# Performance work log

Measured on AMD Instinct MI355X. Metric: run time of the kernel, lower is better.

## Reference

```python
import jax, jax.numpy as jnp
import numpy as np

D_QKV = 64

def setup_inputs() -> dict:
    key = jax.random.key(0)
    k1, k2, k3, k4 = jax.random.split(key, 4)
    B, T, D = 4, 2048, 1024
    x = jax.random.normal(k1, (B, T, D), dtype=jnp.float32)
    Wq = jax.random.normal(k2, (D, D_QKV), dtype=jnp.float32) * (D ** -0.5)
    Wk = jax.random.normal(k3, (D, D_QKV), dtype=jnp.float32) * (D ** -0.5)
    Wv = jax.random.normal(k4, (D, D_QKV), dtype=jnp.float32) * (D ** -0.5)
    return {"x": x, "Wq": Wq, "Wk": Wk, "Wv": Wv}

def reference(x, Wq, Wk, Wv):
    # x: [B, T, D]; single-head causal attention with head dim d_qkv
    T = x.shape[1]
    q = jnp.einsum("btd,de->bte", x, Wq)  # [B, T, d]
    k = jnp.einsum("btd,de->bte", x, Wk)
    v = jnp.einsum("btd,de->bte", x, Wv)
    scores = jnp.einsum("bqe,bke->bqk", q, k) / (D_QKV ** 0.5)  # [B, T, T]
    causal = jnp.tril(jnp.ones((T, T), dtype=bool))
    scores = jnp.where(causal, scores, -jnp.inf)
    attn = jax.nn.softmax(scores, axis=2)
    return jnp.einsum("bqk,bke->bqe", attn, v)  # [B, T, d]
```

## Files before the change

### kernel.cpp

```cpp
#include <hip/hip_runtime.h>
#include <hip/hip_bf16.h>

typedef __hip_bfloat16 bf16;
typedef __bf16 bf16x8 __attribute__((ext_vector_type(8)));
typedef float f32x4 __attribute__((ext_vector_type(4)));
typedef unsigned short u16x8 __attribute__((ext_vector_type(8)));

#define B_SZ   4
#define T_SEQ  2048
#define D_IN   1024
#define D_QKV  64
#define BT     (B_SZ * T_SEQ)
#define PSTR   72

#define GLD_LDS(gp, lp) __builtin_amdgcn_global_load_lds(                     \
    (const __attribute__((address_space(1))) void*)(gp),                      \
    (__attribute__((address_space(3))) void*)(lp), 16, 0, 0)

__global__ __launch_bounds__(256) void wt_prep(
    const float* __restrict__ Wq, const float* __restrict__ Wk,
    const float* __restrict__ Wv, bf16* __restrict__ wt)
{
    __shared__ float ws[64 * 65];
    const int bx = blockIdx.x;
    const int m  = bx >> 4;
    const int k0 = (bx & 15) << 6;
    const float* W = (m == 0) ? Wq : (m == 1) ? Wk : Wv;
    const int tid = threadIdx.x;
    #pragma unroll
    for (int i = 0; i < 16; ++i) {
        const int idx = i * 256 + tid;
        const int kk = idx >> 6, nn = idx & 63;
        ws[kk * 65 + nn] = W[(size_t)(k0 + kk) * D_QKV + nn];
    }
    __syncthreads();
    const int n = tid >> 2, kq = (tid & 3) << 4;
    bf16 tmp[16];
    #pragma unroll
    for (int j = 0; j < 16; ++j)
        tmp[j] = __float2bfloat16(ws[(kq + j) * 65 + n]);
    uint4* dst = (uint4*)(wt + (size_t)(m * 64 + n) * D_IN + k0 + kq);
    dst[0] = ((uint4*)tmp)[0];
    dst[1] = ((uint4*)tmp)[1];
}

__global__ __launch_bounds__(256) void qkv_proj_mfma(
    const float* __restrict__ x, const bf16* __restrict__ wt,
    bf16* __restrict__ qb, bf16* __restrict__ kb, bf16* __restrict__ vt)
{
    __shared__ uint4 As[2][1024];
    __shared__ uint4 Bs[2][768];

    const int tid  = threadIdx.x;
    const int wave = tid >> 6;
    const int lane = tid & 63;
    const int col  = lane & 15;
    const int quad = lane >> 4;
    const int bx   = blockIdx.x;
    const int m0   = (bx >> 1) * 64;
    const int ng   = bx & 1;

    f32x4 acc[6];
    #pragma unroll
    for (int i = 0; i < 6; ++i) acc[i] = (f32x4){0.f, 0.f, 0.f, 0.f};

    auto stage = [&](int it, int buf) {
        const int k0 = it * 64;
        #pragma unroll
        for (int j = 0; j < 7; ++j) {
            const int s = wave + j * 4;
            if (s < 16) {
                const int c = s * 64 + lane;
                const int r = c >> 4;
                const int ccl = ((c & 15) - r) & 15;
                const float* g = x + (size_t)(m0 + r) * D_IN + k0 + ccl * 4;
                GLD_LDS(g, &As[buf][s * 64]);
            } else {
                const int bs = s - 16;
                const int c = bs * 64 + lane;
                const int n = c >> 3;
                const int ccl = ((c & 7) - n) & 7;
                const bf16* g = wt + (size_t)(ng * 96 + n) * D_IN + k0 + ccl * 8;
                GLD_LDS(g, &Bs[buf][bs * 64]);
            }
        }
    };

    stage(0, 0);
    const int r = wave * 16 + col;
    #pragma unroll 1
    for (int it = 0; it < 16; ++it) {
        __syncthreads();
        if (it + 1 < 16) stage(it + 1, (it + 1) & 1);
        const float4* Ac = (const float4*)As[it & 1];
        const uint4*  Bc = Bs[it & 1];
        #pragma unroll
        for (int s = 0; s < 2; ++s) {
            const int ca = s * 8 + quad * 2;
            const float4 a0 = Ac[r * 16 + ((ca + r) & 15)];
            const float4 a1 = Ac[r * 16 + ((ca + 1 + r) & 15)];
            const bf16x8 af = (bf16x8){(__bf16)a0.x, (__bf16)a0.y, (__bf16)a0.z, (__bf16)a0.w,
                                       (__bf16)a1.x, (__bf16)a1.y, (__bf16)a1.z, (__bf16)a1.w};
            #pragma unroll
            for (int i = 0; i < 6; ++i) {
                const int n = i * 16 + col;
                const bf16x8 bfr = __builtin_bit_cast(bf16x8,
                    Bc[n * 8 + ((s * 4 + quad + n) & 7)]);
                acc[i] = __builtin_amdgcn_mfma_f32_16x16x32_bf16(af, bfr, acc[i], 0, 0, 0);
            }
        }
    }

    const int bb = m0 >> 11;
    const int tl = m0 & (T_SEQ - 1);
    #pragma unroll
    for (int i = 0; i < 6; ++i) {
        const int n = ng * 96 + i * 16 + col;
        #pragma unroll
        for (int rr = 0; rr < 4; ++rr) {
            const int row = m0 + wave * 16 + quad * 4 + rr;
            const bf16 vq = __float2bfloat16(acc[i][rr]);
            if (n < 64)       qb[(size_t)row * D_QKV + n] = vq;
            else if (n < 128) kb[(size_t)row * D_QKV + (n - 64)] = vq;
            else              vt[(size_t)bb * D_QKV * T_SEQ + (size_t)(n - 128) * T_SEQ
                                 + (tl + wave * 16 + quad * 4 + rr)] = vq;
        }
    }
}

__global__ __launch_bounds__(256) void attn_kernel(
    const bf16* __restrict__ qb, const bf16* __restrict__ kb,
    const bf16* __restrict__ vt, float* __restrict__ Op, float* __restrict__ lp)
{
    __shared__ uint4 Ks[2][512];
    __shared__ uint4 Vs[2][512];
    __shared__ unsigned short plds[4 * 16 * PSTR];

    const int tid  = threadIdx.x;
    const int wave = tid >> 6;
    const int lane = tid & 63;
    const int col  = lane & 15;
    const int quad = lane >> 4;
    const int bx   = blockIdx.x;
    const int tile    = (bx < 256) ? (127 - (bx >> 2)) : ((bx - 256) >> 2);
    const int quarter = bx & 3;
    const int b    = tile >> 5;
    const int qloc = (tile & 31) * 64;
    const int nch  = (tile & 31) + 1;

    const bf16* kbp = kb + (size_t)b * T_SEQ * D_QKV;
    const bf16* vtp = vt + (size_t)b * D_QKV * T_SEQ;
    const uint4* q4 = (const uint4*)(qb + (size_t)b * T_SEQ * D_QKV);

    const bf16x8 aq0 = __builtin_bit_cast(bf16x8, q4[(qloc + wave * 16 + col) * 8 + quad]);
    const bf16x8 aq1 = __builtin_bit_cast(bf16x8, q4[(qloc + wave * 16 + col) * 8 + 4 + quad]);

    f32x4 o[4];
    float ls[4];
    #pragma unroll
    for (int dt = 0; dt < 4; ++dt) o[dt] = (f32x4){0.f, 0.f, 0.f, 0.f};
    #pragma unroll
    for (int rr = 0; rr < 4; ++rr) ls[rr] = 0.f;

    unsigned short* pl = plds + wave * 16 * PSTR;
    const u16x8* p8 = (const u16x8*)pl;

    auto stage = [&](int c, int buf) {
        const int kb0 = c * 64;
        #pragma unroll
        for (int j = 0; j < 4; ++j) {
            const int s = wave + j * 4;
            if (s < 8) {
                const int ch = s * 64 + lane;
                const int key = ch >> 3;
                const int ccl = ((ch & 7) - key) & 7;
                const bf16* g = kbp + (size_t)(kb0 + key) * D_QKV + ccl * 8;
                GLD_LDS(g, &Ks[buf][s * 64]);
            } else {
                const int vs = s - 8;
                const int ch = vs * 64 + lane;
                const int d = ch >> 3;
                const int ccl = ((ch & 7) - d) & 7;
                const bf16* g = vtp + (size_t)d * T_SEQ + kb0 + ccl * 8;
                GLD_LDS(g, &Vs[buf][vs * 64]);
            }
        }
    };

    if (quarter < nch) stage(quarter, 0);
    int i = 0;
    for (int c = quarter; c < nch; c += 4, ++i) {
        __syncthreads();
        if (c + 4 < nch) stage(c + 4, (i + 1) & 1);
        const uint4* Kc = Ks[i & 1];
        const uint4* Vc = Vs[i & 1];

        f32x4 sc[4];
        #pragma unroll
        for (int nt = 0; nt < 4; ++nt) {
            const int kp = nt * 16 + col;
            const bf16x8 bk0 = __builtin_bit_cast(bf16x8, Kc[kp * 8 + ((quad + kp) & 7)]);
            const bf16x8 bk1 = __builtin_bit_cast(bf16x8, Kc[kp * 8 + ((4 + quad + kp) & 7)]);
            sc[nt] = (f32x4){0.f, 0.f, 0.f, 0.f};
            sc[nt] = __builtin_amdgcn_mfma_f32_16x16x32_bf16(aq0, bk0, sc[nt], 0, 0, 0);
            sc[nt] = __builtin_amdgcn_mfma_f32_16x16x32_bf16(aq1, bk1, sc[nt], 0, 0, 0);
        }

        if (c == nch - 1) {
            #pragma unroll
            for (int nt = 0; nt < 4; ++nt) {
                const int kp = c * 64 + nt * 16 + col;
                #pragma unroll
                for (int rr = 0; rr < 4; ++rr)
                    if (kp > qloc + wave * 16 + quad * 4 + rr) sc[nt][rr] = -INFINITY;
            }
        }

        #pragma unroll
        for (int nt = 0; nt < 4; ++nt) {
            #pragma unroll
            for (int rr = 0; rr < 4; ++rr) {
                const float pv = __expf(sc[nt][rr] * 0.125f);
                ls[rr] += pv;
                pl[(quad * 4 + rr) * PSTR + nt * 16 + col] =
                    __builtin_bit_cast(unsigned short, __float2bfloat16(pv));
            }
        }

        const bf16x8 pa0 = __builtin_bit_cast(bf16x8, p8[col * 9 + quad]);
        const bf16x8 pa1 = __builtin_bit_cast(bf16x8, p8[col * 9 + 4 + quad]);

        #pragma unroll
        for (int dt = 0; dt < 4; ++dt) {
            const int dp = dt * 16 + col;
            const bf16x8 bv0 = __builtin_bit_cast(bf16x8, Vc[dp * 8 + ((quad + dp) & 7)]);
            const bf16x8 bv1 = __builtin_bit_cast(bf16x8, Vc[dp * 8 + ((4 + quad + dp) & 7)]);
            o[dt] = __builtin_amdgcn_mfma_f32_16x16x32_bf16(pa0, bv0, o[dt], 0, 0, 0);
            o[dt] = __builtin_amdgcn_mfma_f32_16x16x32_bf16(pa1, bv1, o[dt], 0, 0, 0);
        }
    }

    #pragma unroll
    for (int rr = 0; rr < 4; ++rr) {
        #pragma unroll
        for (int msk = 1; msk < 16; msk <<= 1)
            ls[rr] += __shfl_xor(ls[rr], msk);
    }

    const int pbase = (tile * 4 + quarter) * 64 + wave * 16;
    #pragma unroll
    for (int dt = 0; dt < 4; ++dt)
        #pragma unroll
        for (int rr = 0; rr < 4; ++rr)
            Op[(size_t)(pbase + quad * 4 + rr) * D_QKV + dt * 16 + col] = o[dt][rr];
    if (col == 0) {
        #pragma unroll
        for (int rr = 0; rr < 4; ++rr)
            lp[pbase + quad * 4 + rr] = ls[rr];
    }
}

__global__ __launch_bounds__(256) void combine_kernel(
    const float* __restrict__ Op, const float* __restrict__ lp,
    float* __restrict__ out)
{
    const int idx = blockIdx.x * 256 + threadIdx.x;
    const int qg = idx >> 6, d = idx & 63;
    const int tile = qg >> 6, qq = qg & 63;
    float s = 0.f, l = 0.f;
    #pragma unroll
    for (int k = 0; k < 4; ++k) {
        s += Op[(size_t)((tile * 4 + k) * 64 + qq) * D_QKV + d];
        l += lp[(tile * 4 + k) * 64 + qq];
    }
    out[(size_t)qg * D_QKV + d] = s / l;
}

extern "C" void kernel_launch(void* const* d_in, const int* in_sizes, int n_in,
                              void* d_out, int out_size, void* d_ws, size_t ws_size,
                              hipStream_t stream) {
    const float* x  = (const float*)d_in[0];
    const float* Wq = (const float*)d_in[1];
    const float* Wk = (const float*)d_in[2];
    const float* Wv = (const float*)d_in[3];
    float* out = (float*)d_out;

    char* ws = (char*)d_ws;
    bf16*  qb = (bf16*)(ws);
    bf16*  kb = (bf16*)(ws + (1u << 20));
    bf16*  vt = (bf16*)(ws + (2u << 20));
    bf16*  wt = (bf16*)(ws + (3u << 20));
    float* Op = (float*)(ws + (4u << 20));
    float* lp = (float*)(ws + (12u << 20));

    wt_prep<<<48, 256, 0, stream>>>(Wq, Wk, Wv, wt);
    qkv_proj_mfma<<<256, 256, 0, stream>>>(x, wt, qb, kb, vt);
    attn_kernel<<<512, 256, 0, stream>>>(qb, kb, vt, Op, lp);
    combine_kernel<<<2048, 256, 0, stream>>>(Op, lp, out);
}
```

Baseline: 110.1 us.

## Split-K QKV projection with 128-row tiles and 128-query attention tiles

The QKV projection now uses 128-row tiles covering all 192 output columns and splits the K dimension into four blocks. This avoids loading x twice, and the fp32 partials are summed in a new combine_qkv kernel that also writes the transposed V. The attention kernel processes two 64-query subtiles per block, reusing each K/V chunk load for both and halving the grid to 256 blocks. In exchange it adds an extra kernel launch, writes and reads about 25 MB of partials, and drops the previous longest-first tile ordering, which risks load imbalance.

```diff
diff --git a/kernel.cpp b/kernel.cpp
--- a/kernel.cpp
+++ b/kernel.cpp
@@ -12,6 +12,7 @@
 #define D_QKV  64
 #define BT     (B_SZ * T_SEQ)
 #define PSTR   72
+#define QS     ((size_t)BT * 192)
 
 #define GLD_LDS(gp, lp) __builtin_amdgcn_global_load_lds(                     \
     (const __attribute__((address_space(1))) void*)(gp),                      \
@@ -46,10 +47,10 @@
 
 __global__ __launch_bounds__(256) void qkv_proj_mfma(
     const float* __restrict__ x, const bf16* __restrict__ wt,
-    bf16* __restrict__ qb, bf16* __restrict__ kb, bf16* __restrict__ vt)
-{
-    __shared__ uint4 As[2][1024];
-    __shared__ uint4 Bs[2][768];
+    float* __restrict__ Pp)
+{
+    __shared__ uint4 As[2][2048];
+    __shared__ uint4 Bs[2][1536];
 
     const int tid  = threadIdx.x;
     const int wave = tid >> 6;
@@ -57,74 +58,113 @@
     const int col  = lane & 15;
     const int quad = lane >> 4;
     const int bx   = blockIdx.x;
-    const int m0   = (bx >> 1) * 64;
-    const int ng   = bx & 1;
-
-    f32x4 acc[6];
-    #pragma unroll
-    for (int i = 0; i < 6; ++i) acc[i] = (f32x4){0.f, 0.f, 0.f, 0.f};
+    const int m0   = (bx >> 2) * 128;
+    const int kq   = bx & 3;
+
+    f32x4 acc[2][12];
+    #pragma unroll
+    for (int mt = 0; mt < 2; ++mt)
+        #pragma unroll
+        for (int i = 0; i < 12; ++i) acc[mt][i] = (f32x4){0.f, 0.f, 0.f, 0.f};
 
     auto stage = [&](int it, int buf) {
-        const int k0 = it * 64;
-        #pragma unroll
-        for (int j = 0; j < 7; ++j) {
+        const int k0 = kq * 256 + it * 64;
+        #pragma unroll
+        for (int j = 0; j < 14; ++j) {
             const int s = wave + j * 4;
-            if (s < 16) {
-                const int c = s * 64 + lane;
-                const int r = c >> 4;
-                const int ccl = ((c & 15) - r) & 15;
-                const float* g = x + (size_t)(m0 + r) * D_IN + k0 + ccl * 4;
+            if (s < 32) {
+                const int o = s * 64 + lane;
+                const int r = o >> 4;
+                const int ch = ((o & 15) - r) & 15;
+                const float* g = x + (size_t)(m0 + r) * D_IN + k0 + ch * 4;
                 GLD_LDS(g, &As[buf][s * 64]);
             } else {
-                const int bs = s - 16;
-                const int c = bs * 64 + lane;
-                const int n = c >> 3;
-                const int ccl = ((c & 7) - n) & 7;
-                const bf16* g = wt + (size_t)(ng * 96 + n) * D_IN + k0 + ccl * 8;
-                GLD_LDS(g, &Bs[buf][bs * 64]);
+                const int o = (s - 32) * 64 + lane;
+                const int n = o >> 3;
+                const int ch = ((o & 7) - n) & 7;
+                const bf16* g = wt + (size_t)n * D_IN + k0 + ch * 8;
+                GLD_LDS(g, &Bs[buf][(s - 32) * 64]);
             }
         }
     };
 
     stage(0, 0);
-    const int r = wave * 16 + col;
     #pragma unroll 1
-    for (int it = 0; it < 16; ++it) {
+    for (int it = 0; it < 4; ++it) {
         __syncthreads();
-        if (it + 1 < 16) stage(it + 1, (it + 1) & 1);
-        const float4* Ac = (const float4*)As[it & 1];
-        const uint4*  Bc = Bs[it & 1];
-        #pragma unroll
-        for (int s = 0; s < 2; ++s) {
-            const int ca = s * 8 + quad * 2;
-            const float4 a0 = Ac[r * 16 + ((ca + r) & 15)];
-            const float4 a1 = Ac[r * 16 + ((ca + 1 + r) & 15)];
-            const bf16x8 af = (bf16x8){(__bf16)a0.x, (__bf16)a0.y, (__bf16)a0.z, (__bf16)a0.w,
-                                       (__bf16)a1.x, (__bf16)a1.y, (__bf16)a1.z, (__bf16)a1.w};
-            #pragma unroll
-            for (int i = 0; i < 6; ++i) {
+        if (it + 1 < 4) stage(it + 1, (it + 1) & 1);
+        const uint4* Ac = As[it & 1];
+        const uint4* Bc = Bs[it & 1];
+        #pragma unroll
+        for (int h = 0; h < 2; ++h) {
+            bf16x8 bf[12];
+            #pragma unroll
+            for (int i = 0; i < 12; ++i) {
                 const int n = i * 16 + col;
-                const bf16x8 bfr = __builtin_bit_cast(bf16x8,
-                    Bc[n * 8 + ((s * 4 + quad + n) & 7)]);
-                acc[i] = __builtin_amdgcn_mfma_f32_16x16x32_bf16(af, bfr, acc[i], 0, 0, 0);
-            }
-        }
-    }
-
-    const int bb = m0 >> 11;
-    const int tl = m0 & (T_SEQ - 1);
-    #pragma unroll
-    for (int i = 0; i < 6; ++i) {
-        const int n = ng * 96 + i * 16 + col;
-        #pragma unroll
-        for (int rr = 0; rr < 4; ++rr) {
-            const int row = m0 + wave * 16 + quad * 4 + rr;
-            const bf16 vq = __float2bfloat16(acc[i][rr]);
-            if (n < 64)       qb[(size_t)row * D_QKV + n] = vq;
-            else if (n < 128) kb[(size_t)row * D_QKV + (n - 64)] = vq;
-            else              vt[(size_t)bb * D_QKV * T_SEQ + (size_t)(n - 128) * T_SEQ
-                                 + (tl + wave * 16 + quad * 4 + rr)] = vq;
-        }
+                bf[i] = __builtin_bit_cast(bf16x8, Bc[n * 8 + ((h * 4 + quad + n) & 7)]);
+            }
+            #pragma unroll
+            for (int mt = 0; mt < 2; ++mt) {
+                const int r = (wave * 2 + mt) * 16 + col;
+                const int ca = h * 8 + quad * 2;
+                const float4 a0 = ((const float4*)Ac)[r * 16 + ((ca + r) & 15)];
+                const float4 a1 = ((const float4*)Ac)[r * 16 + ((ca + 1 + r) & 15)];
+                const bf16x8 af = (bf16x8){(__bf16)a0.x, (__bf16)a0.y, (__bf16)a0.z, (__bf16)a0.w,
+                                           (__bf16)a1.x, (__bf16)a1.y, (__bf16)a1.z, (__bf16)a1.w};
+                #pragma unroll
+                for (int i = 0; i < 12; ++i)
+                    acc[mt][i] = __builtin_amdgcn_mfma_f32_16x16x32_bf16(af, bf[i], acc[mt][i], 0, 0, 0);
+            }
+        }
+    }
+
+    float* P = Pp + (size_t)kq * QS;
+    #pragma unroll
+    for (int mt = 0; mt < 2; ++mt) {
+        const int rowb = m0 + (wave * 2 + mt) * 16 + quad * 4;
+        #pragma unroll
+        for (int i = 0; i < 12; ++i) {
+            const int n = i * 16 + col;
+            #pragma unroll
+            for (int rr = 0; rr < 4; ++rr)
+                P[(size_t)(rowb + rr) * 192 + n] = acc[mt][i][rr];
+        }
+    }
+}
+
+__global__ __launch_bounds__(256) void combine_qkv(
+    const float* __restrict__ Pp, bf16* __restrict__ qb,
+    bf16* __restrict__ kb, bf16* __restrict__ vt)
+{
+    __shared__ float sv[64 * 33];
+    const int t0  = blockIdx.x * 32;
+    const int tid = threadIdx.x;
+
+    #pragma unroll
+    for (int i = 0; i < 16; ++i) {
+        const int idx = i * 256 + tid;
+        const int row = idx >> 7, n = idx & 127;
+        const size_t off = (size_t)(t0 + row) * 192 + n;
+        const float s = Pp[off] + Pp[QS + off] + Pp[2 * QS + off] + Pp[3 * QS + off];
+        const bf16 vq = __float2bfloat16(s);
+        if (n < 64) qb[(size_t)(t0 + row) * D_QKV + n] = vq;
+        else        kb[(size_t)(t0 + row) * D_QKV + (n - 64)] = vq;
+    }
+    #pragma unroll
+    for (int i = 0; i < 8; ++i) {
+        const int idx = i * 256 + tid;
+        const int row = idx >> 6, d = idx & 63;
+        const size_t off = (size_t)(t0 + row) * 192 + 128 + d;
+        sv[d * 33 + row] = Pp[off] + Pp[QS + off] + Pp[2 * QS + off] + Pp[3 * QS + off];
+    }
+    __syncthreads();
+    const int b = t0 >> 11, tl = t0 & (T_SEQ - 1);
+    #pragma unroll
+    for (int i = 0; i < 8; ++i) {
+        const int idx = i * 256 + tid;
+        const int d = idx >> 5, t = idx & 31;
+        vt[(size_t)b * D_QKV * T_SEQ + (size_t)d * T_SEQ + tl + t] =
+            __float2bfloat16(sv[d * 33 + t]);
     }
 }
 
@@ -142,25 +182,34 @@
     const int col  = lane & 15;
     const int quad = lane >> 4;
     const int bx   = blockIdx.x;
-    const int tile    = (bx < 256) ? (127 - (bx >> 2)) : ((bx - 256) >> 2);
+    const int tile    = bx >> 2;
     const int quarter = bx & 3;
-    const int b    = tile >> 5;
-    const int qloc = (tile & 31) * 64;
-    const int nch  = (tile & 31) + 1;
+    const int b    = tile >> 4;
+    const int lt   = tile & 15;
+    const int qg0  = lt * 128;
+    const int nch  = 2 * lt + 2;
 
     const bf16* kbp = kb + (size_t)b * T_SEQ * D_QKV;
     const bf16* vtp = vt + (size_t)b * D_QKV * T_SEQ;
     const uint4* q4 = (const uint4*)(qb + (size_t)b * T_SEQ * D_QKV);
 
-    const bf16x8 aq0 = __builtin_bit_cast(bf16x8, q4[(qloc + wave * 16 + col) * 8 + quad]);
-    const bf16x8 aq1 = __builtin_bit_cast(bf16x8, q4[(qloc + wave * 16 + col) * 8 + 4 + quad]);
-
-    f32x4 o[4];
-    float ls[4];
-    #pragma unroll
-    for (int dt = 0; dt < 4; ++dt) o[dt] = (f32x4){0.f, 0.f, 0.f, 0.f};
-    #pragma unroll
-    for (int rr = 0; rr < 4; ++rr) ls[rr] = 0.f;
+    bf16x8 aq[2][2];
+    #pragma unroll
+    for (int sub = 0; sub < 2; ++sub) {
+        const int row = qg0 + sub * 64 + wave * 16 + col;
+        aq[sub][0] = __builtin_bit_cast(bf16x8, q4[row * 8 + quad]);
+        aq[sub][1] = __builtin_bit_cast(bf16x8, q4[row * 8 + 4 + quad]);
+    }
+
+    f32x4 o[2][4];
+    float ls[2][4];
+    #pragma unroll
+    for (int sub = 0; sub < 2; ++sub)
+        #pragma unroll
+        for (int dt = 0; dt < 4; ++dt) {
+            o[sub][dt] = (f32x4){0.f, 0.f, 0.f, 0.f};
+            ls[sub][dt] = 0.f;
+        }
 
     unsigned short* pl = plds + wave * 16 * PSTR;
     const u16x8* p8 = (const u16x8*)pl;
@@ -171,18 +220,17 @@
         for (int j = 0; j < 4; ++j) {
             const int s = wave + j * 4;
             if (s < 8) {
-                const int ch = s * 64 + lane;
-                const int key = ch >> 3;
-                const int ccl = ((ch & 7) - key) & 7;
-                const bf16* g = kbp + (size_t)(kb0 + key) * D_QKV + ccl * 8;
+                const int o2 = s * 64 + lane;
+                const int key = o2 >> 3;
+                const int ch = ((o2 & 7) - key) & 7;
+                const bf16* g = kbp + (size_t)(kb0 + key) * D_QKV + ch * 8;
                 GLD_LDS(g, &Ks[buf][s * 64]);
             } else {
-                const int vs = s - 8;
-                const int ch = vs * 64 + lane;
-                const int d = ch >> 3;
-                const int ccl = ((ch & 7) - d) & 7;
-                const bf16* g = vtp + (size_t)d * T_SEQ + kb0 + ccl * 8;
-                GLD_LDS(g, &Vs[buf][vs * 64]);
+                const int o2 = (s - 8) * 64 + lane;
+                const int d = o2 >> 3;
+                const int ch = ((o2 & 7) - d) & 7;
+                const bf16* g = vtp + (size_t)d * T_SEQ + kb0 + ch * 8;
+                GLD_LDS(g, &Vs[buf][(s - 8) * 64]);
             }
         }
     };
@@ -195,83 +243,98 @@
         const uint4* Kc = Ks[i & 1];
         const uint4* Vc = Vs[i & 1];
 
-        f32x4 sc[4];
-        #pragma unroll
-        for (int nt = 0; nt < 4; ++nt) {
-            const int kp = nt * 16 + col;
-            const bf16x8 bk0 = __builtin_bit_cast(bf16x8, Kc[kp * 8 + ((quad + kp) & 7)]);
-            const bf16x8 bk1 = __builtin_bit_cast(bf16x8, Kc[kp * 8 + ((4 + quad + kp) & 7)]);
-            sc[nt] = (f32x4){0.f, 0.f, 0.f, 0.f};
-            sc[nt] = __builtin_amdgcn_mfma_f32_16x16x32_bf16(aq0, bk0, sc[nt], 0, 0, 0);
-            sc[nt] = __builtin_amdgcn_mfma_f32_16x16x32_bf16(aq1, bk1, sc[nt], 0, 0, 0);
-        }
-
-        if (c == nch - 1) {
-            #pragma unroll
-            for (int nt = 0; nt < 4; ++nt) {
-                const int kp = c * 64 + nt * 16 + col;
-                #pragma unroll
-                for (int rr = 0; rr < 4; ++rr)
-                    if (kp > qloc + wave * 16 + quad * 4 + rr) sc[nt][rr] = -INFINITY;
-            }
-        }
-
-        #pragma unroll
-        for (int nt = 0; nt < 4; ++nt) {
-            #pragma unroll
-            for (int rr = 0; rr < 4; ++rr) {
-                const float pv = __expf(sc[nt][rr] * 0.125f);
-                ls[rr] += pv;
-                pl[(quad * 4 + rr) * PSTR + nt * 16 + col] =
-                    __builtin_bit_cast(unsigned short, __float2bfloat16(pv));
-            }
-        }
-
-        const bf16x8 pa0 = __builtin_bit_cast(bf16x8, p8[col * 9 + quad]);
-        const bf16x8 pa1 = __builtin_bit_cast(bf16x8, p8[col * 9 + 4 + quad]);
-
+        bf16x8 bv0[4], bv1[4];
         #pragma unroll
         for (int dt = 0; dt < 4; ++dt) {
             const int dp = dt * 16 + col;
-            const bf16x8 bv0 = __builtin_bit_cast(bf16x8, Vc[dp * 8 + ((quad + dp) & 7)]);
-            const bf16x8 bv1 = __builtin_bit_cast(bf16x8, Vc[dp * 8 + ((4 + quad + dp) & 7)]);
-            o[dt] = __builtin_amdgcn_mfma_f32_16x16x32_bf16(pa0, bv0, o[dt], 0, 0, 0);
-            o[dt] = __builtin_amdgcn_mfma_f32_16x16x32_bf16(pa1, bv1, o[dt], 0, 0, 0);
-        }
-    }
-
-    #pragma unroll
-    for (int rr = 0; rr < 4; ++rr) {
-        #pragma unroll
-        for (int msk = 1; msk < 16; msk <<= 1)
-            ls[rr] += __shfl_xor(ls[rr], msk);
-    }
-
-    const int pbase = (tile * 4 + quarter) * 64 + wave * 16;
-    #pragma unroll
-    for (int dt = 0; dt < 4; ++dt)
-        #pragma unroll
-        for (int rr = 0; rr < 4; ++rr)
-            Op[(size_t)(pbase + quad * 4 + rr) * D_QKV + dt * 16 + col] = o[dt][rr];
-    if (col == 0) {
-        #pragma unroll
-        for (int rr = 0; rr < 4; ++rr)
-            lp[pbase + quad * 4 + rr] = ls[rr];
-    }
-}
-
-__global__ __launch_bounds__(256) void combine_kernel(
+            bv0[dt] = __builtin_bit_cast(bf16x8, Vc[dp * 8 + ((quad + dp) & 7)]);
+            bv1[dt] = __builtin_bit_cast(bf16x8, Vc[dp * 8 + ((4 + quad + dp) & 7)]);
+        }
+
+        #pragma unroll
+        for (int sub = 0; sub < 2; ++sub) {
+            if (sub == 0 && c == nch - 1) continue;
+
+            f32x4 sc[4];
+            #pragma unroll
+            for (int nt = 0; nt < 4; ++nt) {
+                const int kp = nt * 16 + col;
+                const bf16x8 bk0 = __builtin_bit_cast(bf16x8, Kc[kp * 8 + ((quad + kp) & 7)]);
+                const bf16x8 bk1 = __builtin_bit_cast(bf16x8, Kc[kp * 8 + ((4 + quad + kp) & 7)]);
+                sc[nt] = (f32x4){0.f, 0.f, 0.f, 0.f};
+                sc[nt] = __builtin_amdgcn_mfma_f32_16x16x32_bf16(aq[sub][0], bk0, sc[nt], 0, 0, 0);
+                sc[nt] = __builtin_amdgcn_mfma_f32_16x16x32_bf16(aq[sub][1], bk1, sc[nt], 0, 0, 0);
+            }
+
+            if (c == nch - 2 + sub) {
+                #pragma unroll
+                for (int nt = 0; nt < 4; ++nt) {
+                    const int kp = c * 64 + nt * 16 + col;
+                    #pragma unroll
+                    for (int rr = 0; rr < 4; ++rr)
+                        if (kp > qg0 + sub * 64 + wave * 16 + quad * 4 + rr)
+                            sc[nt][rr] = -INFINITY;
+                }
+            }
+
+            #pragma unroll
+            for (int nt = 0; nt < 4; ++nt) {
+                #pragma unroll
+                for (int rr = 0; rr < 4; ++rr) {
+                    const float pv = __expf(sc[nt][rr] * 0.125f);
+                    ls[sub][rr] += pv;
+                    pl[(quad * 4 + rr) * PSTR + nt * 16 + col] =
+                        __builtin_bit_cast(unsigned short, __float2bfloat16(pv));
+                }
+            }
+            const bf16x8 pa0 = __builtin_bit_cast(bf16x8, p8[col * 9 + quad]);
+            const bf16x8 pa1 = __builtin_bit_cast(bf16x8, p8[col * 9 + 4 + quad]);
+            #pragma unroll
+            for (int dt = 0; dt < 4; ++dt) {
+                o[sub][dt] = __builtin_amdgcn_mfma_f32_16x16x32_bf16(pa0, bv0[dt], o[sub][dt], 0, 0, 0);
+                o[sub][dt] = __builtin_amdgcn_mfma_f32_16x16x32_bf16(pa1, bv1[dt], o[sub][dt], 0, 0, 0);
+            }
+        }
+    }
+
+    #pragma unroll
+    for (int sub = 0; sub < 2; ++sub)
+        #pragma unroll
+        for (int rr = 0; rr < 4; ++rr) {
+            #pragma unroll
+            for (int msk = 1; msk < 16; msk <<= 1)
+                ls[sub][rr] += __shfl_xor(ls[sub][rr], msk);
+        }
+
+    const int pbase = (tile * 4 + quarter) * 128;
+    #pragma unroll
+    for (int sub = 0; sub < 2; ++sub) {
+        #pragma unroll
+        for (int dt = 0; dt < 4; ++dt)
+            #pragma unroll
+            for (int rr = 0; rr < 4; ++rr)
+                Op[(size_t)(pbase + sub * 64 + wave * 16 + quad * 4 + rr) * D_QKV
+                   + dt * 16 + col] = o[sub][dt][rr];
+        if (col == 0) {
+            #pragma unroll
+            for (int rr = 0; rr < 4; ++rr)
+                lp[pbase + sub * 64 + wave * 16 + quad * 4 + rr] = ls[sub][rr];
+        }
+    }
+}
+
+__global__ __launch_bounds__(256) void combine_attn(
     const float* __restrict__ Op, const float* __restrict__ lp,
     float* __restrict__ out)
 {
     const int idx = blockIdx.x * 256 + threadIdx.x;
     const int qg = idx >> 6, d = idx & 63;
-    const int tile = qg >> 6, qq = qg & 63;
+    const int tile = qg >> 7, rr = qg & 127;
     float s = 0.f, l = 0.f;
     #pragma unroll
     for (int k = 0; k < 4; ++k) {
-        s += Op[(size_t)((tile * 4 + k) * 64 + qq) * D_QKV + d];
-        l += lp[(tile * 4 + k) * 64 + qq];
+        s += Op[(size_t)((tile * 4 + k) * 128 + rr) * D_QKV + d];
+        l += lp[(tile * 4 + k) * 128 + rr];
     }
     out[(size_t)qg * D_QKV + d] = s / l;
 }
@@ -290,11 +353,13 @@
     bf16*  kb = (bf16*)(ws + (1u << 20));
     bf16*  vt = (bf16*)(ws + (2u << 20));
     bf16*  wt = (bf16*)(ws + (3u << 20));
-    float* Op = (float*)(ws + (4u << 20));
-    float* lp = (float*)(ws + (12u << 20));
+    float* Pp = (float*)(ws + (4u << 20));
+    float* Op = (float*)(ws + (32u << 20));
+    float* lp = (float*)(ws + (40u << 20));
 
     wt_prep<<<48, 256, 0, stream>>>(Wq, Wk, Wv, wt);
-    qkv_proj_mfma<<<256, 256, 0, stream>>>(x, wt, qb, kb, vt);
-    attn_kernel<<<512, 256, 0, stream>>>(qb, kb, vt, Op, lp);
-    combine_kernel<<<2048, 256, 0, stream>>>(Op, lp, out);
-}
+    qkv_proj_mfma<<<256, 256, 0, stream>>>(x, wt, Pp);
+    combine_qkv<<<256, 256, 0, stream>>>(Pp, qb, kb, vt);
+    attn_kernel<<<256, 256, 0, stream>>>(qb, kb, vt, Op, lp);
+    combine_attn<<<2048, 256, 0, stream>>>(Op, lp, out);
+}
```

New measurement: 116.6 us. 5.9% more time.

## Process two query sub-tiles per block to reuse staged K/V tiles

Applied to the files above, without the earlier changes.

Each attention block now handles 128 query rows (two 64-row sub-tiles) instead of 64, so each staged K/V chunk and the V fragments held in registers feed two sets of score and PV MFMAs. The grid halves to 256 blocks and the split-K combine indexing is adjusted to 128-row tiles. This aims to cut global-to-LDS traffic and staging overhead per unit of work. In exchange it raises register pressure, drops the reversed tile ordering that balanced the causal workload, and leaves fewer blocks to spread across CUs.

```diff
diff --git a/kernel.cpp b/kernel.cpp
--- a/kernel.cpp
+++ b/kernel.cpp
@@ -142,25 +142,34 @@
     const int col  = lane & 15;
     const int quad = lane >> 4;
     const int bx   = blockIdx.x;
-    const int tile    = (bx < 256) ? (127 - (bx >> 2)) : ((bx - 256) >> 2);
+    const int tile    = bx >> 2;
     const int quarter = bx & 3;
-    const int b    = tile >> 5;
-    const int qloc = (tile & 31) * 64;
-    const int nch  = (tile & 31) + 1;
+    const int b    = tile >> 4;
+    const int lt   = tile & 15;
+    const int qg0  = lt * 128;
+    const int nch  = 2 * lt + 2;
 
     const bf16* kbp = kb + (size_t)b * T_SEQ * D_QKV;
     const bf16* vtp = vt + (size_t)b * D_QKV * T_SEQ;
     const uint4* q4 = (const uint4*)(qb + (size_t)b * T_SEQ * D_QKV);
 
-    const bf16x8 aq0 = __builtin_bit_cast(bf16x8, q4[(qloc + wave * 16 + col) * 8 + quad]);
-    const bf16x8 aq1 = __builtin_bit_cast(bf16x8, q4[(qloc + wave * 16 + col) * 8 + 4 + quad]);
-
-    f32x4 o[4];
-    float ls[4];
-    #pragma unroll
-    for (int dt = 0; dt < 4; ++dt) o[dt] = (f32x4){0.f, 0.f, 0.f, 0.f};
-    #pragma unroll
-    for (int rr = 0; rr < 4; ++rr) ls[rr] = 0.f;
+    bf16x8 aq[2][2];
+    #pragma unroll
+    for (int sub = 0; sub < 2; ++sub) {
+        const int row = qg0 + sub * 64 + wave * 16 + col;
+        aq[sub][0] = __builtin_bit_cast(bf16x8, q4[row * 8 + quad]);
+        aq[sub][1] = __builtin_bit_cast(bf16x8, q4[row * 8 + 4 + quad]);
+    }
+
+    f32x4 o[2][4];
+    float ls[2][4];
+    #pragma unroll
+    for (int sub = 0; sub < 2; ++sub)
+        #pragma unroll
+        for (int dt = 0; dt < 4; ++dt) {
+            o[sub][dt] = (f32x4){0.f, 0.f, 0.f, 0.f};
+            ls[sub][dt] = 0.f;
+        }
 
     unsigned short* pl = plds + wave * 16 * PSTR;
     const u16x8* p8 = (const u16x8*)pl;
@@ -171,18 +180,17 @@
         for (int j = 0; j < 4; ++j) {
             const int s = wave + j * 4;
             if (s < 8) {
-                const int ch = s * 64 + lane;
-                const int key = ch >> 3;
-                const int ccl = ((ch & 7) - key) & 7;
-                const bf16* g = kbp + (size_t)(kb0 + key) * D_QKV + ccl * 8;
+                const int o2 = s * 64 + lane;
+                const int key = o2 >> 3;
+                const int ch = ((o2 & 7) - key) & 7;
+                const bf16* g = kbp + (size_t)(kb0 + key) * D_QKV + ch * 8;
                 GLD_LDS(g, &Ks[buf][s * 64]);
             } else {
-                const int vs = s - 8;
-                const int ch = vs * 64 + lane;
-                const int d = ch >> 3;
-                const int ccl = ((ch & 7) - d) & 7;
-                const bf16* g = vtp + (size_t)d * T_SEQ + kb0 + ccl * 8;
-                GLD_LDS(g, &Vs[buf][vs * 64]);
+                const int o2 = (s - 8) * 64 + lane;
+                const int d = o2 >> 3;
+                const int ch = ((o2 & 7) - d) & 7;
+                const bf16* g = vtp + (size_t)d * T_SEQ + kb0 + ch * 8;
+                GLD_LDS(g, &Vs[buf][(s - 8) * 64]);
             }
         }
     };
@@ -195,83 +203,98 @@
         const uint4* Kc = Ks[i & 1];
         const uint4* Vc = Vs[i & 1];
 
-        f32x4 sc[4];
-        #pragma unroll
-        for (int nt = 0; nt < 4; ++nt) {
-            const int kp = nt * 16 + col;
-            const bf16x8 bk0 = __builtin_bit_cast(bf16x8, Kc[kp * 8 + ((quad + kp) & 7)]);
-            const bf16x8 bk1 = __builtin_bit_cast(bf16x8, Kc[kp * 8 + ((4 + quad + kp) & 7)]);
-            sc[nt] = (f32x4){0.f, 0.f, 0.f, 0.f};
-            sc[nt] = __builtin_amdgcn_mfma_f32_16x16x32_bf16(aq0, bk0, sc[nt], 0, 0, 0);
-            sc[nt] = __builtin_amdgcn_mfma_f32_16x16x32_bf16(aq1, bk1, sc[nt], 0, 0, 0);
-        }
-
-        if (c == nch - 1) {
-            #pragma unroll
-            for (int nt = 0; nt < 4; ++nt) {
-                const int kp = c * 64 + nt * 16 + col;
-                #pragma unroll
-                for (int rr = 0; rr < 4; ++rr)
-                    if (kp > qloc + wave * 16 + quad * 4 + rr) sc[nt][rr] = -INFINITY;
-            }
-        }
-
-        #pragma unroll
-        for (int nt = 0; nt < 4; ++nt) {
-            #pragma unroll
-            for (int rr = 0; rr < 4; ++rr) {
-                const float pv = __expf(sc[nt][rr] * 0.125f);
-                ls[rr] += pv;
-                pl[(quad * 4 + rr) * PSTR + nt * 16 + col] =
-                    __builtin_bit_cast(unsigned short, __float2bfloat16(pv));
-            }
-        }
-
-        const bf16x8 pa0 = __builtin_bit_cast(bf16x8, p8[col * 9 + quad]);
-        const bf16x8 pa1 = __builtin_bit_cast(bf16x8, p8[col * 9 + 4 + quad]);
-
+        bf16x8 bv0[4], bv1[4];
         #pragma unroll
         for (int dt = 0; dt < 4; ++dt) {
             const int dp = dt * 16 + col;
-            const bf16x8 bv0 = __builtin_bit_cast(bf16x8, Vc[dp * 8 + ((quad + dp) & 7)]);
-            const bf16x8 bv1 = __builtin_bit_cast(bf16x8, Vc[dp * 8 + ((4 + quad + dp) & 7)]);
-            o[dt] = __builtin_amdgcn_mfma_f32_16x16x32_bf16(pa0, bv0, o[dt], 0, 0, 0);
-            o[dt] = __builtin_amdgcn_mfma_f32_16x16x32_bf16(pa1, bv1, o[dt], 0, 0, 0);
-        }
-    }
-
-    #pragma unroll
-    for (int rr = 0; rr < 4; ++rr) {
-        #pragma unroll
-        for (int msk = 1; msk < 16; msk <<= 1)
-            ls[rr] += __shfl_xor(ls[rr], msk);
-    }
-
-    const int pbase = (tile * 4 + quarter) * 64 + wave * 16;
-    #pragma unroll
-    for (int dt = 0; dt < 4; ++dt)
-        #pragma unroll
-        for (int rr = 0; rr < 4; ++rr)
-            Op[(size_t)(pbase + quad * 4 + rr) * D_QKV + dt * 16 + col] = o[dt][rr];
-    if (col == 0) {
-        #pragma unroll
-        for (int rr = 0; rr < 4; ++rr)
-            lp[pbase + quad * 4 + rr] = ls[rr];
-    }
-}
-
-__global__ __launch_bounds__(256) void combine_kernel(
+            bv0[dt] = __builtin_bit_cast(bf16x8, Vc[dp * 8 + ((quad + dp) & 7)]);
+            bv1[dt] = __builtin_bit_cast(bf16x8, Vc[dp * 8 + ((4 + quad + dp) & 7)]);
+        }
+
+        #pragma unroll
+        for (int sub = 0; sub < 2; ++sub) {
+            if (sub == 0 && c == nch - 1) continue;
+
+            f32x4 sc[4];
+            #pragma unroll
+            for (int nt = 0; nt < 4; ++nt) {
+                const int kp = nt * 16 + col;
+                const bf16x8 bk0 = __builtin_bit_cast(bf16x8, Kc[kp * 8 + ((quad + kp) & 7)]);
+                const bf16x8 bk1 = __builtin_bit_cast(bf16x8, Kc[kp * 8 + ((4 + quad + kp) & 7)]);
+                sc[nt] = (f32x4){0.f, 0.f, 0.f, 0.f};
+                sc[nt] = __builtin_amdgcn_mfma_f32_16x16x32_bf16(aq[sub][0], bk0, sc[nt], 0, 0, 0);
+                sc[nt] = __builtin_amdgcn_mfma_f32_16x16x32_bf16(aq[sub][1], bk1, sc[nt], 0, 0, 0);
+            }
+
+            if (c == nch - 2 + sub) {
+                #pragma unroll
+                for (int nt = 0; nt < 4; ++nt) {
+                    const int kp = c * 64 + nt * 16 + col;
+                    #pragma unroll
+                    for (int rr = 0; rr < 4; ++rr)
+                        if (kp > qg0 + sub * 64 + wave * 16 + quad * 4 + rr)
+                            sc[nt][rr] = -INFINITY;
+                }
+            }
+
+            #pragma unroll
+            for (int nt = 0; nt < 4; ++nt) {
+                #pragma unroll
+                for (int rr = 0; rr < 4; ++rr) {
+                    const float pv = __expf(sc[nt][rr] * 0.125f);
+                    ls[sub][rr] += pv;
+                    pl[(quad * 4 + rr) * PSTR + nt * 16 + col] =
+                        __builtin_bit_cast(unsigned short, __float2bfloat16(pv));
+                }
+            }
+            const bf16x8 pa0 = __builtin_bit_cast(bf16x8, p8[col * 9 + quad]);
+            const bf16x8 pa1 = __builtin_bit_cast(bf16x8, p8[col * 9 + 4 + quad]);
+            #pragma unroll
+            for (int dt = 0; dt < 4; ++dt) {
+                o[sub][dt] = __builtin_amdgcn_mfma_f32_16x16x32_bf16(pa0, bv0[dt], o[sub][dt], 0, 0, 0);
+                o[sub][dt] = __builtin_amdgcn_mfma_f32_16x16x32_bf16(pa1, bv1[dt], o[sub][dt], 0, 0, 0);
+            }
+        }
+    }
+
+    #pragma unroll
+    for (int sub = 0; sub < 2; ++sub)
+        #pragma unroll
+        for (int rr = 0; rr < 4; ++rr) {
+            #pragma unroll
+            for (int msk = 1; msk < 16; msk <<= 1)
+                ls[sub][rr] += __shfl_xor(ls[sub][rr], msk);
+        }
+
+    const int pbase = (tile * 4 + quarter) * 128;
+    #pragma unroll
+    for (int sub = 0; sub < 2; ++sub) {
+        #pragma unroll
+        for (int dt = 0; dt < 4; ++dt)
+            #pragma unroll
+            for (int rr = 0; rr < 4; ++rr)
+                Op[(size_t)(pbase + sub * 64 + wave * 16 + quad * 4 + rr) * D_QKV
+                   + dt * 16 + col] = o[sub][dt][rr];
+        if (col == 0) {
+            #pragma unroll
+            for (int rr = 0; rr < 4; ++rr)
+                lp[pbase + sub * 64 + wave * 16 + quad * 4 + rr] = ls[sub][rr];
+        }
+    }
+}
+
+__global__ __launch_bounds__(256) void combine_attn(
     const float* __restrict__ Op, const float* __restrict__ lp,
     float* __restrict__ out)
 {
     const int idx = blockIdx.x * 256 + threadIdx.x;
     const int qg = idx >> 6, d = idx & 63;
-    const int tile = qg >> 6, qq = qg & 63;
+    const int tile = qg >> 7, rr = qg & 127;
     float s = 0.f, l = 0.f;
     #pragma unroll
     for (int k = 0; k < 4; ++k) {
-        s += Op[(size_t)((tile * 4 + k) * 64 + qq) * D_QKV + d];
-        l += lp[(tile * 4 + k) * 64 + qq];
+        s += Op[(size_t)((tile * 4 + k) * 128 + rr) * D_QKV + d];
+        l += lp[(tile * 4 + k) * 128 + rr];
     }
     out[(size_t)qg * D_QKV + d] = s / l;
 }
@@ -295,6 +318,6 @@
 
     wt_prep<<<48, 256, 0, stream>>>(Wq, Wk, Wv, wt);
     qkv_proj_mfma<<<256, 256, 0, stream>>>(x, wt, qb, kb, vt);
-    attn_kernel<<<512, 256, 0, stream>>>(qb, kb, vt, Op, lp);
-    combine_kernel<<<2048, 256, 0, stream>>>(Op, lp, out);
-}
+    attn_kernel<<<256, 256, 0, stream>>>(qb, kb, vt, Op, lp);
+    combine_attn<<<2048, 256, 0, stream>>>(Op, lp, out);
+}
```

Measured after the change: 115.9 us. +5.3%, slower.
